# Kernel tuning notes

Hardware: AMD Instinct MI355X
Metric: run time of the kernel (lower is better)

The kernel has to match this reference:

```python
import jax, jax.numpy as jnp
import numpy as np

WORD_VOCAB = 100000
TAG_VOCAB = 50
WD = 300
TD = 100
EMB = WD + TD          # 400: LSTM input size AND hidden size
H = EMB
L = 512


def setup_inputs() -> dict:
    key = jax.random.key(0)
    ks = jax.random.split(key, 16)
    def p(k, shape):
        return jax.random.normal(k, shape, dtype=jnp.float32) * 0.05
    return {
        "words_idx_tensor": jax.random.randint(ks[0], (1, L), 0, WORD_VOCAB),
        "tags_idx_tensor": jax.random.randint(ks[1], (1, L), 0, TAG_VOCAB),
        "max_length": L,
        "word_emb": p(ks[2], (WORD_VOCAB, WD)),
        "tag_emb": p(ks[3], (TAG_VOCAB, TD)),
        # stacked [fwd, bwd] directions per layer (PyTorch LSTM gate order i,f,g,o)
        "w_ih_l0": p(ks[4], (2, 4 * H, EMB)),
        "w_hh_l0": p(ks[5], (2, 4 * H, H)),
        "b_ih_l0": p(ks[6], (2, 4 * H)),
        "b_hh_l0": p(ks[7], (2, 4 * H)),
        "w_ih_l1": p(ks[8], (2, 4 * H, 2 * H)),
        "w_hh_l1": p(ks[9], (2, 4 * H, H)),
        "b_ih_l1": p(ks[10], (2, 4 * H)),
        "b_hh_l1": p(ks[11], (2, 4 * H)),
        "fc1_w": p(ks[12], (1, 4 * H)),
        "fc1_b": p(ks[13], (1,)),
    }


def _lstm_dir(x, w_ih, w_hh, b_ih, b_hh, reverse):
    # x: [T, in]. Precompute input projections once (hoisted out of scan).
    xi = x @ w_ih.T + b_ih + b_hh  # [T, 4H]
    Hn = w_hh.shape[1]

    def step(carry, g_in):
        h, c = carry
        g = g_in + h @ w_hh.T
        i, f, gg, o = jnp.split(g, 4, axis=-1)
        c = jax.nn.sigmoid(f) * c + jax.nn.sigmoid(i) * jnp.tanh(gg)
        h = jax.nn.sigmoid(o) * jnp.tanh(c)
        return (h, c), h

    init = (jnp.zeros((Hn,), x.dtype), jnp.zeros((Hn,), x.dtype))
    _, hs = jax.lax.scan(step, init, xi, reverse=reverse)
    return hs  # [T, H]


def _bilstm(x, w_ih, w_hh, b_ih, b_hh):
    fwd = _lstm_dir(x, w_ih[0], w_hh[0], b_ih[0], b_hh[0], False)
    bwd = _lstm_dir(x, w_ih[1], w_hh[1], b_ih[1], b_hh[1], True)
    return jnp.concatenate([fwd, bwd], axis=-1)  # [T, 2H]


def reference(words_idx_tensor, tags_idx_tensor, max_length, word_emb, tag_emb,
              w_ih_l0, w_hh_l0, b_ih_l0, b_hh_l0,
              w_ih_l1, w_hh_l1, b_ih_l1, b_hh_l1,
              fc1_w, fc1_b):
    # Embedding lookup + concat; batch dim of size 1 squeezed (torch's
    # view(shape[1], shape[0], -1) yields [L, 1, emb] for the LSTM).
    x = jnp.concatenate([word_emb[words_idx_tensor[0]],
                         tag_emb[tags_idx_tensor[0]]], axis=-1)  # [L, EMB]

    h = _bilstm(x, w_ih_l0, w_hh_l0, b_ih_l0, b_hh_l0)   # [L, 2H]
    h = _bilstm(h, w_ih_l1, w_hh_l1, b_ih_l1, b_hh_l1)   # [L, 2H]

    # Pairwise edge scores: tanh(W @ [h_i; h_j] + b).
    # Split W into head/dep halves -> two small GEMMs + broadcast outer-sum,
    # avoiding the O(L^2 * 4H) concatenated feature tensor.
    two_h = fc1_w.shape[1] // 2
    s = h @ fc1_w[:, :two_h].T   # [L, 1]
    t = h @ fc1_w[:, two_h:].T   # [L, 1]
    scores = jnp.tanh(s[:, None, :] + t[None, :, :] + fc1_b)  # [L, L, 1]
    # torch stacks (i outer, j inner) -> [L*L, 1, 1]
    return scores.reshape(max_length * max_length, 1, 1)
```

## Files before the change

kernel.cpp:

```cpp
#include <hip/hip_runtime.h>

#define SEQ 512
#define HID 400
#define GATES 1600
#define E1 800
#define TEAM 10
#define RECGRID 160

__device__ __forceinline__ float bf2f(unsigned short u) {
    return __uint_as_float(((unsigned)u) << 16);
}
__device__ __forceinline__ unsigned short f2bf(float f) {
    unsigned u = __float_as_uint(f);
    u += 0x7FFFu + ((u >> 16) & 1u);
    return (unsigned short)(u >> 16);
}
__device__ __forceinline__ float sigm(float x) { return 1.f / (1.f + __expf(-x)); }
__device__ __forceinline__ float tanh_f(float x) {
    float xc = fminf(fmaxf(x, -15.f), 15.f);
    float e = __expf(2.f * xc);
    return (e - 1.f) / (e + 1.f);
}
__device__ __forceinline__ float loadx(const void* p, size_t i, int isbf) {
    return isbf ? bf2f(((const unsigned short*)p)[i]) : ((const float*)p)[i];
}

__global__ void detect_kernel(const unsigned short* __restrict__ wemb,
                              unsigned* __restrict__ dtf) {
    __shared__ int cnt;
    if (threadIdx.x == 0) cnt = 0;
    __syncthreads();
    int pass = 0;
    for (int i = 0; i < 8; ++i) {
        unsigned short u = wemb[threadIdx.x * 8 + i];
        int e = (u >> 7) & 0xFF;
        pass += (e >= 100 && e <= 130) ? 1 : 0;
    }
    atomicAdd(&cnt, pass);
    __syncthreads();
    if (threadIdx.x == 0) *dtf = (cnt >= 1843) ? 1u : 0u;
}

__global__ void embed_kernel(const int* __restrict__ words, const int* __restrict__ tags,
                             const void* __restrict__ wemb, const void* __restrict__ temb,
                             float* __restrict__ x ,
                             const unsigned* __restrict__ dtf) {
    int t = blockIdx.x;
    int w = words[t], g = tags[t];
    int isbf = (int)*dtf;
    for (int k = threadIdx.x; k < HID; k += blockDim.x) {
        float v = (k < 300) ? loadx(wemb, (size_t)w * 300 + k, isbf)
                            : loadx(temb, (size_t)g * 100 + (k - 300), isbf);
        x[(size_t)t * HID + k] = v;
    }
}

__global__ __launch_bounds__(256) void proj_kernel(
        const void* __restrict__ Araw, int tagged,
        const void* __restrict__ Wraw ,
        const void* __restrict__ bihRaw, const void* __restrict__ bhhRaw,
        float* __restrict__ xi ,
        int K, const unsigned* __restrict__ dtf) {
    const int isbf = (int)*dtf;
    __shared__ float As[16][132];
    __shared__ float Ws[16][68];
    int tid = threadIdx.x;
    int t0 = blockIdx.x * 128, n0 = blockIdx.y * 64, dir = blockIdx.z;
    int arow = tid >> 1, akoff = (tid & 1) * 8;
    int wrow = tid >> 2, wkoff = (tid & 3) * 4;
    int tx = (tid & 15) * 4;
    int ty = (tid >> 4) * 8;

    const float* Af = (const float*)Araw + (size_t)(t0 + arow) * K + akoff;
    const unsigned long long* At = (const unsigned long long*)Araw +
                                   (size_t)(t0 + arow) * K + akoff;
    size_t wbase = (size_t)(dir * GATES + n0 + wrow) * K + wkoff;
    const float* Wf = (const float*)Wraw + wbase;
    const unsigned short* Wh = (const unsigned short*)Wraw + wbase;

    float acc[8][4] = {};
    for (int k0 = 0; k0 < K; k0 += 16) {
        float av8[8];
        if (tagged) {
            ulonglong2 q0 = *(const ulonglong2*)(At + k0);
            ulonglong2 q1 = *(const ulonglong2*)(At + k0 + 2);
            ulonglong2 q2 = *(const ulonglong2*)(At + k0 + 4);
            ulonglong2 q3 = *(const ulonglong2*)(At + k0 + 6);
            av8[0] = __uint_as_float((unsigned)q0.x); av8[1] = __uint_as_float((unsigned)q0.y);
            av8[2] = __uint_as_float((unsigned)q1.x); av8[3] = __uint_as_float((unsigned)q1.y);
            av8[4] = __uint_as_float((unsigned)q2.x); av8[5] = __uint_as_float((unsigned)q2.y);
            av8[6] = __uint_as_float((unsigned)q3.x); av8[7] = __uint_as_float((unsigned)q3.y);
        } else {
            float4 a0 = *(const float4*)(Af + k0);
            float4 a1 = *(const float4*)(Af + k0 + 4);
            av8[0] = a0.x; av8[1] = a0.y; av8[2] = a0.z; av8[3] = a0.w;
            av8[4] = a1.x; av8[5] = a1.y; av8[6] = a1.z; av8[7] = a1.w;
        }
        float4 wv;
        if (isbf) {
            ushort4 w4 = *(const ushort4*)(Wh + k0);
            wv = make_float4(bf2f(w4.x), bf2f(w4.y), bf2f(w4.z), bf2f(w4.w));
        } else {
            wv = *(const float4*)(Wf + k0);
        }
        __syncthreads();
#pragma unroll
        for (int i = 0; i < 8; ++i) As[akoff + i][arow] = av8[i];
        Ws[wkoff + 0][wrow] = wv.x; Ws[wkoff + 1][wrow] = wv.y;
        Ws[wkoff + 2][wrow] = wv.z; Ws[wkoff + 3][wrow] = wv.w;
        __syncthreads();
#pragma unroll
        for (int kk = 0; kk < 16; ++kk) {
            float4 alo = *(const float4*)&As[kk][ty];
            float4 ahi = *(const float4*)&As[kk][ty + 4];
            float4 w4  = *(const float4*)&Ws[kk][tx];
            float av[8] = {alo.x, alo.y, alo.z, alo.w, ahi.x, ahi.y, ahi.z, ahi.w};
            float wvv[4] = {w4.x, w4.y, w4.z, w4.w};
#pragma unroll
            for (int i = 0; i < 8; ++i)
#pragma unroll
                for (int j = 0; j < 4; ++j)
                    acc[i][j] = fmaf(av[i], wvv[j], acc[i][j]);
        }
    }
    float bias[4];
#pragma unroll
    for (int j = 0; j < 4; ++j) {
        int n = n0 + tx + j;
        bias[j] = loadx(bihRaw, dir * GATES + n, isbf) + loadx(bhhRaw, dir * GATES + n, isbf);
    }
    float* xout = xi + (size_t)dir * SEQ * GATES;
#pragma unroll
    for (int i = 0; i < 8; ++i) {
        int t = t0 + ty + i;
        float4 o = make_float4(acc[i][0] + bias[0], acc[i][1] + bias[1],
                               acc[i][2] + bias[2], acc[i][3] + bias[3]);
        *(float4*)&xout[(size_t)t * GATES + n0 + tx] = o;
    }
}

struct SyncArea { unsigned cnt[8]; unsigned claim[2]; unsigned pad[6]; };

template <int ISBF>
__global__ __launch_bounds__(512, 2) void rec_kernel(
        const float* __restrict__ xi ,
        const void* __restrict__ whhRaw ,
        unsigned long long* __restrict__ hx  ,
        unsigned long long* __restrict__ hx2 ,
        unsigned tagbase, SyncArea* __restrict__ sy,
        const unsigned* __restrict__ dtf) {
    if (*(volatile const unsigned*)dtf != (unsigned)ISBF) return;

    int tid = threadIdx.x;
    __shared__ int role[2];
    if (tid == 0) {
        unsigned xcd = __builtin_amdgcn_s_getreg((3 << 11) | 20) & 0xFu;
        unsigned rank = atomicAdd(&sy->cnt[xcd], 1u);
        unsigned group = rank / TEAM;
        unsigned key = 1u + xcd * 64u + group;
        if ((rank % TEAM) == TEAM - 1) {
            unsigned prev = atomicCAS(&sy->claim[0], 0u, key);
            if (prev != 0u) atomicCAS(&sy->claim[1], 0u, key);
        }
        int dir = -1;
        while (dir < 0) {
            unsigned c0 = __hip_atomic_load(&sy->claim[0], __ATOMIC_RELAXED,
                                            __HIP_MEMORY_SCOPE_AGENT);
            unsigned c1 = __hip_atomic_load(&sy->claim[1], __ATOMIC_RELAXED,
                                            __HIP_MEMORY_SCOPE_AGENT);
            if (c0 == key) dir = 0;
            else if (c1 == key) dir = 1;
            else if (c0 != 0u && c1 != 0u) dir = 2;
        }
        role[0] = dir;
        role[1] = (int)(rank % TEAM);
    }
    __syncthreads();
    const int dir = role[0];
    const int wg  = role[1];
    if (dir == 2) return;

    int chunk = tid & 15;
    int rg    = tid >> 4;
    const int dirHID = dir * HID;

    __shared__ __align__(16) float hbuf[HID];
    __shared__ __align__(16) float partials[160][20];
    __shared__ __align__(16) float gates[160];

    unsigned pk[5][13];
    float    wf[5][25];
#pragma unroll
    for (int r = 0; r < 5; ++r) {
        int lr = rg * 5 + r;
        int jj = lr >> 2, gg = lr & 3;
        int grow = gg * HID + wg * 40 + jj;
        size_t base = ((size_t)dir * GATES + grow) * HID + chunk * 25;
        if (ISBF) {
            const unsigned short* p = (const unsigned short*)whhRaw + base;
#pragma unroll
            for (int c2 = 0; c2 < 12; ++c2)
                pk[r][c2] = ((unsigned)p[2 * c2 + 1] << 16) | (unsigned)p[2 * c2];
            pk[r][12] = ((unsigned)p[24]) << 16;
        } else {
            const float* p = (const float*)whhRaw + base;
#pragma unroll
            for (int c = 0; c < 25; ++c) wf[r][c] = p[c];
        }
    }

    int xrow = 0;
    if (tid < 160) { int jj = tid >> 2, gg = tid & 3; xrow = gg * HID + wg * 40 + jj; }
    const float* xibase = xi + (size_t)dir * SEQ * GATES;
    float cstate = 0.f;
    size_t myelem = dirHID + wg * 40 + tid;

#pragma unroll 1
    for (int k = 0; k < SEQ; ++k) {
        int t = dir ? (SEQ - 1 - k) : k;
        float xiv = 0.f;
        if (tid < 160) xiv = xibase[(size_t)t * GATES + xrow];

        if (k > 0) {
            int tprev = dir ? (t + 1) : (t - 1);
            if (tid < HID) {
                const unsigned want = tagbase + (unsigned)k;
                size_t eidx = (size_t)tprev * E1 + dirHID + tid;
                const volatile unsigned long long* p =
                    (const volatile unsigned long long*)&hx[eidx];
                unsigned long long w;
                int spin = 0;
                for (;;) {
                    w = *p;
                    if ((unsigned)(w >> 32) == want) break;
                    if (++spin >= 24) {
                        w = __hip_atomic_load(&hx2[eidx], __ATOMIC_RELAXED,
                                              __HIP_MEMORY_SCOPE_AGENT);
                        if ((unsigned)(w >> 32) == want) break;
                        spin = 0;
                    }
                }
                hbuf[tid] = __uint_as_float((unsigned)w);
            }
        } else {
            if (tid < HID) hbuf[tid] = 0.f;
        }
        __syncthreads();

        float acc[5] = {0.f, 0.f, 0.f, 0.f, 0.f};
        if (ISBF) {
#pragma unroll
            for (int c2 = 0; c2 < 12; ++c2) {
                float h0 = hbuf[chunk * 25 + 2 * c2];
                float h1 = hbuf[chunk * 25 + 2 * c2 + 1];
#pragma unroll
                for (int r = 0; r < 5; ++r) {
                    unsigned u = pk[r][c2];
                    acc[r] = fmaf(__uint_as_float(u << 16), h0, acc[r]);
                    acc[r] = fmaf(__uint_as_float(u & 0xffff0000u), h1, acc[r]);
                }
            }
            float h24 = hbuf[chunk * 25 + 24];
#pragma unroll
            for (int r = 0; r < 5; ++r)
                acc[r] = fmaf(__uint_as_float(pk[r][12]), h24, acc[r]);
        } else {
#pragma unroll
            for (int c = 0; c < 25; ++c) {
                float hv = hbuf[chunk * 25 + c];
#pragma unroll
                for (int r = 0; r < 5; ++r)
                    acc[r] = fmaf(wf[r][c], hv, acc[r]);
            }
        }
#pragma unroll
        for (int r = 0; r < 5; ++r) partials[rg * 5 + r][chunk] = acc[r];
        __syncthreads();

        if (tid < 160) {
            const float4* pr = (const float4*)&partials[tid][0];
            float4 p0 = pr[0], p1 = pr[1], p2 = pr[2], p3 = pr[3];
            float s = p0.x + p0.y + p0.z + p0.w
                    + p1.x + p1.y + p1.z + p1.w
                    + p2.x + p2.y + p2.z + p2.w
                    + p3.x + p3.y + p3.z + p3.w;
            gates[tid] = s + xiv;
        }
        __syncthreads();

        if (tid < 40) {
            float4 g4 = *(const float4*)&gates[tid * 4];
            float ig = sigm(g4.x), fg = sigm(g4.y), cg = tanh_f(g4.z), og = sigm(g4.w);
            cstate = fg * cstate + ig * cg;
            float hv = og * tanh_f(cstate);
            unsigned long long w =
                ((unsigned long long)(tagbase + (unsigned)k + 1u) << 32) |
                (unsigned long long)(unsigned)__float_as_uint(hv);
            size_t eidx = (size_t)t * E1 + myelem;
            *(volatile unsigned long long*)&hx[eidx] = w;
            __hip_atomic_store(&hx2[eidx], w, __ATOMIC_RELAXED,
                               __HIP_MEMORY_SCOPE_AGENT);
        }
    }
}

__global__ void st_kernel(const unsigned long long* __restrict__ h1x ,
                          const void* __restrict__ fw ,
                          float* __restrict__ sv, float* __restrict__ tv,
                          const unsigned* __restrict__ dtf) {
    int i = blockIdx.x;
    int lane = threadIdx.x;
    int isbf = (int)*dtf;
    float s = 0.f, t = 0.f;
    for (int j = lane; j < E1; j += 64) {
        float hv = __uint_as_float((unsigned)h1x[(size_t)i * E1 + j]);
        s += hv * loadx(fw, j, isbf);
        t += hv * loadx(fw, E1 + j, isbf);
    }
#pragma unroll
    for (int o = 32; o > 0; o >>= 1) {
        s += __shfl_xor(s, o, 64);
        t += __shfl_xor(t, o, 64);
    }
    if (lane == 0) { sv[i] = s; tv[i] = t; }
}

__global__ void scores_kernel(const float* __restrict__ sv, const float* __restrict__ tv,
                              const void* __restrict__ fb, void* __restrict__ out,
                              const unsigned* __restrict__ dtf) {
    int idx = blockIdx.x * blockDim.x + threadIdx.x;
    int i = idx >> 9, j = idx & 511;
    int isbf = (int)*dtf;
    float v = tanh_f(sv[i] + tv[j] + loadx(fb, 0, isbf));
    if (isbf) ((unsigned short*)out)[idx] = f2bf(v);
    else      ((float*)out)[idx] = v;
}

static constexpr size_t OFF_X    = 0;
static constexpr size_t OFF_XI   = 819200;
static constexpr size_t OFF_SV   = 7372800;
static constexpr size_t OFF_TV   = 7374848;
static constexpr size_t OFF_DTF  = 7376896;
static constexpr size_t OFF_SYNC = 7376960;
static constexpr size_t OFF_HX   = 7377216;
static constexpr size_t OFF_HX2  = 10654016;

extern "C" void kernel_launch(void* const* d_in, const int* in_sizes, int n_in,
                              void* d_out, int out_size, void* d_ws, size_t ws_size,
                              hipStream_t stream) {
    const int* words = (const int*)d_in[0];
    const int* tags  = (const int*)d_in[1];
    const void* wemb = d_in[3];
    const void* temb = d_in[4];
    const void* wih0 = d_in[5];
    const void* whh0 = d_in[6];
    const void* bih0 = d_in[7];
    const void* bhh0 = d_in[8];
    const void* wih1 = d_in[9];
    const void* whh1 = d_in[10];
    const void* bih1 = d_in[11];
    const void* bhh1 = d_in[12];
    const void* fw   = d_in[13];
    const void* fb   = d_in[14];

    char* ws = (char*)d_ws;
    float* x               = (float*)(ws + OFF_X);
    float* xi              = (float*)(ws + OFF_XI);
    float* sv              = (float*)(ws + OFF_SV);
    float* tv              = (float*)(ws + OFF_TV);
    unsigned* dtf          = (unsigned*)(ws + OFF_DTF);
    SyncArea* sync0        = (SyncArea*)(ws + OFF_SYNC);
    SyncArea* sync1        = (SyncArea*)(ws + OFF_SYNC + 64);
    unsigned long long* hx  = (unsigned long long*)(ws + OFF_HX);
    unsigned long long* hx2 = (unsigned long long*)(ws + OFF_HX2);

    hipMemsetAsync(ws + OFF_SYNC, 0, 128, stream);
    detect_kernel<<<1, 256, 0, stream>>>((const unsigned short*)wemb, dtf);
    embed_kernel<<<SEQ, 128, 0, stream>>>(words, tags, wemb, temb, x, dtf);

    proj_kernel<<<dim3(4, 25, 2), 256, 0, stream>>>(x, 0, wih0, bih0, bhh0, xi, HID, dtf);
    rec_kernel<1><<<RECGRID, 512, 0, stream>>>(xi, whh0, hx, hx2, 0u, sync0, dtf);
    rec_kernel<0><<<RECGRID, 512, 0, stream>>>(xi, whh0, hx, hx2, 0u, sync0, dtf);

    proj_kernel<<<dim3(4, 25, 2), 256, 0, stream>>>(hx, 1, wih1, bih1, bhh1, xi, E1, dtf);
    rec_kernel<1><<<RECGRID, 512, 0, stream>>>(xi, whh1, hx, hx2, 512u, sync1, dtf);
    rec_kernel<0><<<RECGRID, 512, 0, stream>>>(xi, whh1, hx, hx2, 512u, sync1, dtf);

    st_kernel<<<SEQ, 64, 0, stream>>>(hx, fw, sv, tv, dtf);
    scores_kernel<<<(SEQ * SEQ) / 256, 256, 0, stream>>>(sv, tv, fb, d_out, dtf);
}
```

Baseline: 1.999 ms.

## Prefetch input projections in chunks to shared memory and drop duplicate h store

The recurrent kernel now stages the precomputed input-projection gates for 8 timesteps at a time into a double-buffered shared array. Each prefetch is issued while the recurrent matvec runs, which takes the per-step global load off the critical path. It also removes the second agent-scope atomic mirror buffer for hidden states, so each step does one store and the consumer spins on a plain volatile load. Relying only on volatile polling across XCDs risks slower visibility of hidden states or even a hang if the volatile load is cached non-coherently.

```diff
diff --git a/kernel.cpp b/kernel.cpp
--- a/kernel.cpp
+++ b/kernel.cpp
@@ -6,6 +6,7 @@
 #define E1 800
 #define TEAM 10
 #define RECGRID 160
+#define XCH 8
 
 __device__ __forceinline__ float bf2f(unsigned short u) {
     return __uint_as_float(((unsigned)u) << 16);
@@ -145,8 +146,7 @@
 __global__ __launch_bounds__(512, 2) void rec_kernel(
         const float* __restrict__ xi ,
         const void* __restrict__ whhRaw ,
-        unsigned long long* __restrict__ hx  ,
-        unsigned long long* __restrict__ hx2 ,
+        unsigned long long* __restrict__ hx ,
         unsigned tagbase, SyncArea* __restrict__ sy,
         const unsigned* __restrict__ dtf) {
     if (*(volatile const unsigned*)dtf != (unsigned)ISBF) return;
@@ -180,13 +180,14 @@
     const int wg  = role[1];
     if (dir == 2) return;
 
-    int chunk = tid & 15;
-    int rg    = tid >> 4;
+    const int chunk = tid & 15;
+    const int rg    = tid >> 4;
     const int dirHID = dir * HID;
 
     __shared__ __align__(16) float hbuf[HID];
     __shared__ __align__(16) float partials[160][20];
     __shared__ __align__(16) float gates[160];
+    __shared__ __align__(16) float xibuf[2][XCH][160];
 
     unsigned pk[5][13];
     float    wf[5][25];
@@ -209,43 +210,55 @@
         }
     }
 
-    int xrow = 0;
-    if (tid < 160) { int jj = tid >> 2, gg = tid & 3; xrow = gg * HID + wg * 40 + jj; }
     const float* xibase = xi + (size_t)dir * SEQ * GATES;
+#pragma unroll
+    for (int u = 0; u < 3; ++u) {
+        int idx = tid + u * 512;
+        if (idx < XCH * 160) {
+            int s = idx / 160, rem = idx - s * 160;
+            int G = rem / 40, j = rem - G * 40;
+            int ts = dir ? (SEQ - 1 - s) : s;
+            xibuf[0][s][rem] = xibase[(size_t)ts * GATES + G * HID + wg * 40 + j];
+        }
+    }
+
     float cstate = 0.f;
-    size_t myelem = dirHID + wg * 40 + tid;
+    size_t myelem = (size_t)dirHID + wg * 40 + tid;
 
 #pragma unroll 1
     for (int k = 0; k < SEQ; ++k) {
         int t = dir ? (SEQ - 1 - k) : k;
-        float xiv = 0.f;
-        if (tid < 160) xiv = xibase[(size_t)t * GATES + xrow];
 
         if (k > 0) {
-            int tprev = dir ? (t + 1) : (t - 1);
             if (tid < HID) {
                 const unsigned want = tagbase + (unsigned)k;
-                size_t eidx = (size_t)tprev * E1 + dirHID + tid;
+                int tprev = dir ? (t + 1) : (t - 1);
                 const volatile unsigned long long* p =
-                    (const volatile unsigned long long*)&hx[eidx];
+                    (const volatile unsigned long long*)&hx[(size_t)tprev * E1 + dirHID + tid];
                 unsigned long long w;
-                int spin = 0;
-                for (;;) {
-                    w = *p;
-                    if ((unsigned)(w >> 32) == want) break;
-                    if (++spin >= 24) {
-                        w = __hip_atomic_load(&hx2[eidx], __ATOMIC_RELAXED,
-                                              __HIP_MEMORY_SCOPE_AGENT);
-                        if ((unsigned)(w >> 32) == want) break;
-                        spin = 0;
-                    }
-                }
+                do { w = *p; } while ((unsigned)(w >> 32) != want);
                 hbuf[tid] = __uint_as_float((unsigned)w);
             }
         } else {
             if (tid < HID) hbuf[tid] = 0.f;
         }
         __syncthreads();
+
+        float pf[3] = {0.f, 0.f, 0.f};
+        const bool fetch = ((k & 7) == 0) && (k + XCH < SEQ);
+        if (fetch) {
+#pragma unroll
+            for (int u = 0; u < 3; ++u) {
+                int idx = tid + u * 512;
+                if (idx < XCH * 160) {
+                    int s = idx / 160, rem = idx - s * 160;
+                    int G = rem / 40, j = rem - G * 40;
+                    int ks = k + XCH + s;
+                    int ts = dir ? (SEQ - 1 - ks) : ks;
+                    pf[u] = xibase[(size_t)ts * GATES + G * HID + wg * 40 + j];
+                }
+            }
+        }
 
         float acc[5] = {0.f, 0.f, 0.f, 0.f, 0.f};
         if (ISBF) {
@@ -275,6 +288,18 @@
         }
 #pragma unroll
         for (int r = 0; r < 5; ++r) partials[rg * 5 + r][chunk] = acc[r];
+
+        if (fetch) {
+            int nb = ((k >> 3) + 1) & 1;
+#pragma unroll
+            for (int u = 0; u < 3; ++u) {
+                int idx = tid + u * 512;
+                if (idx < XCH * 160) {
+                    int s = idx / 160, rem = idx - s * 160;
+                    xibuf[nb][s][rem] = pf[u];
+                }
+            }
+        }
         __syncthreads();
 
         if (tid < 160) {
@@ -284,7 +309,7 @@
                     + p1.x + p1.y + p1.z + p1.w
                     + p2.x + p2.y + p2.z + p2.w
                     + p3.x + p3.y + p3.z + p3.w;
-            gates[tid] = s + xiv;
+            gates[tid] = s + xibuf[(k >> 3) & 1][k & 7][(tid & 3) * 40 + (tid >> 2)];
         }
         __syncthreads();
 
@@ -295,11 +320,8 @@
             float hv = og * tanh_f(cstate);
             unsigned long long w =
                 ((unsigned long long)(tagbase + (unsigned)k + 1u) << 32) |
-                (unsigned long long)(unsigned)__float_as_uint(hv);
-            size_t eidx = (size_t)t * E1 + myelem;
-            *(volatile unsigned long long*)&hx[eidx] = w;
-            __hip_atomic_store(&hx2[eidx], w, __ATOMIC_RELAXED,
-                               __HIP_MEMORY_SCOPE_AGENT);
+                (unsigned long long)__float_as_uint(hv);
+            *(volatile unsigned long long*)&hx[(size_t)t * E1 + myelem] = w;
         }
     }
 }
@@ -343,7 +365,6 @@
 static constexpr size_t OFF_DTF  = 7376896;
 static constexpr size_t OFF_SYNC = 7376960;
 static constexpr size_t OFF_HX   = 7377216;
-static constexpr size_t OFF_HX2  = 10654016;
 
 extern "C" void kernel_launch(void* const* d_in, const int* in_sizes, int n_in,
                               void* d_out, int out_size, void* d_ws, size_t ws_size,
@@ -371,20 +392,19 @@
     unsigned* dtf          = (unsigned*)(ws + OFF_DTF);
     SyncArea* sync0        = (SyncArea*)(ws + OFF_SYNC);
     SyncArea* sync1        = (SyncArea*)(ws + OFF_SYNC + 64);
-    unsigned long long* hx  = (unsigned long long*)(ws + OFF_HX);
-    unsigned long long* hx2 = (unsigned long long*)(ws + OFF_HX2);
+    unsigned long long* hx = (unsigned long long*)(ws + OFF_HX);
 
     hipMemsetAsync(ws + OFF_SYNC, 0, 128, stream);
     detect_kernel<<<1, 256, 0, stream>>>((const unsigned short*)wemb, dtf);
     embed_kernel<<<SEQ, 128, 0, stream>>>(words, tags, wemb, temb, x, dtf);
 
     proj_kernel<<<dim3(4, 25, 2), 256, 0, stream>>>(x, 0, wih0, bih0, bhh0, xi, HID, dtf);
-    rec_kernel<1><<<RECGRID, 512, 0, stream>>>(xi, whh0, hx, hx2, 0u, sync0, dtf);
-    rec_kernel<0><<<RECGRID, 512, 0, stream>>>(xi, whh0, hx, hx2, 0u, sync0, dtf);
+    rec_kernel<1><<<RECGRID, 512, 0, stream>>>(xi, whh0, hx, 0u, sync0, dtf);
+    rec_kernel<0><<<RECGRID, 512, 0, stream>>>(xi, whh0, hx, 0u, sync0, dtf);
 
     proj_kernel<<<dim3(4, 25, 2), 256, 0, stream>>>(hx, 1, wih1, bih1, bhh1, xi, E1, dtf);
-    rec_kernel<1><<<RECGRID, 512, 0, stream>>>(xi, whh1, hx, hx2, 512u, sync1, dtf);
-    rec_kernel<0><<<RECGRID, 512, 0, stream>>>(xi, whh1, hx, hx2, 512u, sync1, dtf);
+    rec_kernel<1><<<RECGRID, 512, 0, stream>>>(xi, whh1, hx, 512u, sync1, dtf);
+    rec_kernel<0><<<RECGRID, 512, 0, stream>>>(xi, whh1, hx, 512u, sync1, dtf);
 
     st_kernel<<<SEQ, 64, 0, stream>>>(hx, fw, sv, tv, dtf);
     scores_kernel<<<(SEQ * SEQ) / 256, 256, 0, stream>>>(sv, tv, fb, d_out, dtf);
```

After: 2.011 ms. Within noise of the previous version (+0.6%).
